# Kernel optimization log

Measured on AMD Instinct MI355X. Metric: run time of the kernel, lower is better.

The kernel has to match this reference:

```python
import jax, jax.numpy as jnp
import numpy as np

D_PRIME = 512
D = 2048
CLASSES = 4


def setup_inputs() -> dict:
    key = jax.random.key(0)
    k1, k2, k3, k4 = jax.random.split(key, 4)
    N = 32768
    V_prime = jax.random.normal(k1, (N, D), dtype=jnp.float32)
    U_t = jax.random.normal(k2, (D_PRIME, D), dtype=jnp.float32)
    W_mta = jax.random.normal(k3, (1, D_PRIME), dtype=jnp.float32)
    W = jax.random.normal(k4, (CLASSES, D), dtype=jnp.float32)
    return {"V_prime": V_prime, "U_t": U_t, "W_mta": W_mta, "W": W}


def reference(V_prime, U_t, W_mta, W):
    # [D_prime, N] = tanh(U_t @ V'^T)
    tanh_scores = jnp.tanh(U_t @ V_prime.T)
    # attention over instances: [1, N]
    a = jax.nn.softmax(W_mta @ tanh_scores, axis=1)
    # weighted sum pooling: [D]
    t = jnp.sum(a.T * V_prime, axis=0)
    # final linear: [1, classes]
    l = (W @ t).reshape(1, CLASSES)
    return l
```

## Files before the change

### kernel.cpp

```cpp
#include <hip/hip_runtime.h>

#define N_INST 32768
#define DIM    2048
#define DP     512
#define NCLS   4

typedef _Float16 half4_t __attribute__((ext_vector_type(4)));
typedef _Float16 half8_t __attribute__((ext_vector_type(8)));
typedef float    float4_t __attribute__((ext_vector_type(4)));

#define OFF_VHI   0ull
#define OFF_UHI   (OFF_VHI  + (size_t)N_INST*DIM*2)
#define OFF_S     (OFF_UHI  + (size_t)DP*DIM*2)
#define OFF_STAT  (OFF_S    + (size_t)N_INST*4)
#define OFF_PART  (OFF_STAT + 256ull)
#define OFF_T     (OFF_PART + 256ull*DIM*4)

#define GLOAD_LDS16(g, l) __builtin_amdgcn_global_load_lds( \
    (__attribute__((address_space(1))) void*)(g),           \
    (__attribute__((address_space(3))) void*)(l), 16, 0, 0)

__device__ __forceinline__ float tanh_fast(float x) {
  float e = __expf(2.0f * x);
  return 1.0f - 2.0f / (e + 1.0f);
}

__global__ __launch_bounds__(256) void k_cvt(const float4* __restrict__ in,
                                             half8_t* __restrict__ out) {
  int i = blockIdx.x * 256 + threadIdx.x;
  float4 a = in[2 * i], b = in[2 * i + 1];
  half8_t h;
  h[0] = (_Float16)a.x; h[1] = (_Float16)a.y;
  h[2] = (_Float16)a.z; h[3] = (_Float16)a.w;
  h[4] = (_Float16)b.x; h[5] = (_Float16)b.y;
  h[6] = (_Float16)b.z; h[7] = (_Float16)b.w;
  out[i] = h;
}

__global__ __launch_bounds__(256) void k_score_gemm(
    const _Float16* __restrict__ Uhi, const _Float16* __restrict__ Vhi,
    const float* __restrict__ Wmta, float* __restrict__ s) {
  __shared__ _Float16 lA[128 * 32];
  __shared__ _Float16 lB[128 * 32];

  const int tid = threadIdx.x;
  const int lane = tid & 63;
  const int wv = tid >> 6;
  const int waveM = wv >> 1;
  const int waveN = wv & 1;
  const int quad = lane >> 4;
  const int col = lane & 15;
  const int mb = blockIdx.x & 3;
  const int nb = blockIdx.x >> 2;

  const int aRow0 = mb * 128;
  const int bRow0 = nb * 128;

  float4_t acc[4][4];
  const float4_t z4 = {0.f, 0.f, 0.f, 0.f};
  for (int i = 0; i < 4; i++)
    for (int j = 0; j < 4; j++) acc[i][j] = z4;

  for (int k0 = 0; k0 < DIM; k0 += 32) {
    for (int it = 0; it < 2; ++it) {
      const int slot = it * 256 + tid;
      const int r = slot >> 2;
      const int c = (slot & 3) << 3;
      const int lbase = (it * 256 + (wv << 6)) << 3;
      GLOAD_LDS16(Uhi + (size_t)(aRow0 + r) * DIM + k0 + c, &lA[lbase]);
      GLOAD_LDS16(Vhi + (size_t)(bRow0 + r) * DIM + k0 + c, &lB[lbase]);
    }
    __syncthreads();

    half8_t af[4], bf[4];
    for (int mi = 0; mi < 4; mi++) {
      const int row = waveM * 64 + mi * 16 + col;
      af[mi] = *(const half8_t*)&lA[row * 32 + quad * 8];
    }
    for (int ni = 0; ni < 4; ni++) {
      const int row = waveN * 64 + ni * 16 + col;
      bf[ni] = *(const half8_t*)&lB[row * 32 + quad * 8];
    }
    for (int mi = 0; mi < 4; mi++)
      for (int ni = 0; ni < 4; ni++)
        acc[mi][ni] = __builtin_amdgcn_mfma_f32_16x16x32_f16(af[mi], bf[ni], acc[mi][ni], 0, 0, 0);
    __syncthreads();
  }

  for (int ni = 0; ni < 4; ni++) {
    float v = 0.0f;
    for (int mi = 0; mi < 4; mi++) {
      const int jb = aRow0 + waveM * 64 + mi * 16 + quad * 4;
      union { float4_t v4; float f[4]; } u;
      u.v4 = acc[mi][ni];
      for (int r = 0; r < 4; r++)
        v += Wmta[jb + r] * tanh_fast(u.f[r]);
    }
    v += __shfl_xor(v, 16);
    v += __shfl_xor(v, 32);
    if (quad == 0) {
      const int n = bRow0 + waveN * 64 + ni * 16 + col;
      atomicAdd(&s[n], v);
    }
  }
}

__global__ __launch_bounds__(1024) void k_stats(const float* __restrict__ s,
                                                float* __restrict__ stats) {
  const int tid = threadIdx.x;
  const int lane = tid & 63;
  const int wv = tid >> 6;
  __shared__ float sm[16];
  __shared__ float bb;
  const float4* s4 = (const float4*)s;

  float m = -3.4e38f;
  for (int i = tid; i < N_INST / 4; i += 1024) {
    float4 v = s4[i];
    m = fmaxf(m, fmaxf(fmaxf(v.x, v.y), fmaxf(v.z, v.w)));
  }
  for (int o = 32; o > 0; o >>= 1) m = fmaxf(m, __shfl_xor(m, o));
  if (lane == 0) sm[wv] = m;
  __syncthreads();
  if (tid == 0) {
    float mm = sm[0];
    for (int w = 1; w < 16; w++) mm = fmaxf(mm, sm[w]);
    bb = mm;
  }
  __syncthreads();
  const float mx = bb;

  float p = 0.0f;
  for (int i = tid; i < N_INST / 4; i += 1024) {
    float4 v = s4[i];
    p += __expf(v.x - mx) + __expf(v.y - mx) + __expf(v.z - mx) + __expf(v.w - mx);
  }
  for (int o = 32; o > 0; o >>= 1) p += __shfl_xor(p, o);
  if (lane == 0) sm[wv] = p;
  __syncthreads();
  if (tid == 0) {
    float sum = 0.0f;
    for (int w = 0; w < 16; w++) sum += sm[w];
    stats[0] = mx;
    stats[1] = 1.0f / sum;
  }
}

__global__ __launch_bounds__(256) void k_pool(const _Float16* __restrict__ Vhi,
                                              const float* __restrict__ s,
                                              const float* __restrict__ stats,
                                              float* __restrict__ part) {
  const int tid = threadIdx.x;
  const float mx = stats[0], inv = stats[1];
  const int n0 = blockIdx.x * 128;
  float acc[8] = {0.f, 0.f, 0.f, 0.f, 0.f, 0.f, 0.f, 0.f};
  for (int r = 0; r < 128; ++r) {
    const int n = n0 + r;
    const float w = __expf(s[n] - mx) * inv;
    if (w > 1e-12f) {
      half8_t v = *(const half8_t*)&Vhi[(size_t)n * DIM + tid * 8];
#pragma unroll
      for (int j = 0; j < 8; ++j) acc[j] += w * (float)v[j];
    }
  }
  float* dst = &part[(size_t)blockIdx.x * DIM + tid * 8];
  *(float4*)(dst + 0) = make_float4(acc[0], acc[1], acc[2], acc[3]);
  *(float4*)(dst + 4) = make_float4(acc[4], acc[5], acc[6], acc[7]);
}

__global__ __launch_bounds__(256) void k_reduce(const float* __restrict__ part,
                                                float* __restrict__ t) {
  const int d = blockIdx.x * 256 + threadIdx.x;
  float acc = 0.f;
  for (int b = 0; b < 256; ++b) acc += part[(size_t)b * DIM + d];
  t[d] = acc;
}

__global__ __launch_bounds__(256) void k_final(const float* __restrict__ W,
                                               const float* __restrict__ t,
                                               float* __restrict__ out) {
  const int wv = threadIdx.x >> 6;
  const int lane = threadIdx.x & 63;
  float p = 0.0f;
  for (int d = lane; d < DIM; d += 64) p += W[wv * DIM + d] * t[d];
  for (int o = 32; o > 0; o >>= 1) p += __shfl_xor(p, o);
  if (lane == 0) out[wv] = p;
}

extern "C" void kernel_launch(void* const* d_in, const int* in_sizes, int n_in,
                              void* d_out, int out_size, void* d_ws, size_t ws_size,
                              hipStream_t stream) {
  const float* Vp   = (const float*)d_in[0];
  const float* Ut   = (const float*)d_in[1];
  const float* Wmta = (const float*)d_in[2];
  const float* W    = (const float*)d_in[3];
  float* out = (float*)d_out;

  char* ws = (char*)d_ws;
  _Float16* Vhi  = (_Float16*)(ws + OFF_VHI);
  _Float16* Uhi  = (_Float16*)(ws + OFF_UHI);
  float*    sBuf = (float*)(ws + OFF_S);
  float*    stat = (float*)(ws + OFF_STAT);
  float*    partB= (float*)(ws + OFF_PART);
  float*    tBuf = (float*)(ws + OFF_T);

  hipMemsetAsync(sBuf, 0, (size_t)N_INST * 4, stream);

  k_cvt<<<(N_INST * DIM / 8) / 256, 256, 0, stream>>>((const float4*)Vp, (half8_t*)Vhi);
  k_cvt<<<(DP * DIM / 8) / 256, 256, 0, stream>>>((const float4*)Ut, (half8_t*)Uhi);
  k_score_gemm<<<(DP / 128) * (N_INST / 128), 256, 0, stream>>>(Uhi, Vhi, Wmta, sBuf);
  k_stats<<<1, 1024, 0, stream>>>(sBuf, stat);
  k_pool<<<N_INST / 128, 256, 0, stream>>>(Vhi, sBuf, stat, partB);
  k_reduce<<<DIM / 256, 256, 0, stream>>>(partB, tBuf);
  k_final<<<1, 256, 0, stream>>>(W, tBuf, out);
}
```

Before: 540.9 us.

## Fuse V fp16 conversion into score GEMM and pool, single-pass softmax stats

Removes the standalone pass that converted the large V matrix to fp16. The score GEMM now loads fp32 V tiles into swizzled LDS and converts them to fp16 in registers, and the pooling kernel reads fp32 V directly. The softmax statistics kernel computes max and sum in one online pass. This trades a full read/write of V for more bytes per GEMM tile load, double the LDS footprint for B, and more pool read traffic.

```diff
diff --git a/kernel.cpp b/kernel.cpp
--- a/kernel.cpp
+++ b/kernel.cpp
@@ -5,12 +5,10 @@
 #define DP     512
 #define NCLS   4
 
-typedef _Float16 half4_t __attribute__((ext_vector_type(4)));
 typedef _Float16 half8_t __attribute__((ext_vector_type(8)));
 typedef float    float4_t __attribute__((ext_vector_type(4)));
 
-#define OFF_VHI   0ull
-#define OFF_UHI   (OFF_VHI  + (size_t)N_INST*DIM*2)
+#define OFF_UHI   0ull
 #define OFF_S     (OFF_UHI  + (size_t)DP*DIM*2)
 #define OFF_STAT  (OFF_S    + (size_t)N_INST*4)
 #define OFF_PART  (OFF_STAT + 256ull)
@@ -38,10 +36,10 @@
 }
 
 __global__ __launch_bounds__(256) void k_score_gemm(
-    const _Float16* __restrict__ Uhi, const _Float16* __restrict__ Vhi,
+    const _Float16* __restrict__ Uhi, const float* __restrict__ V,
     const float* __restrict__ Wmta, float* __restrict__ s) {
   __shared__ _Float16 lA[128 * 32];
-  __shared__ _Float16 lB[128 * 32];
+  __shared__ float    lB[128 * 32];
 
   const int tid = threadIdx.x;
   const int lane = tid & 63;
@@ -61,14 +59,22 @@
   for (int i = 0; i < 4; i++)
     for (int j = 0; j < 4; j++) acc[i][j] = z4;
 
+  const int aR = tid >> 2;
+  const int aC = (tid & 3) << 3;
+  const int bR = tid >> 3;
+  const int bG0 = tid & 7;
+
   for (int k0 = 0; k0 < DIM; k0 += 32) {
     for (int it = 0; it < 2; ++it) {
-      const int slot = it * 256 + tid;
-      const int r = slot >> 2;
-      const int c = (slot & 3) << 3;
-      const int lbase = (it * 256 + (wv << 6)) << 3;
-      GLOAD_LDS16(Uhi + (size_t)(aRow0 + r) * DIM + k0 + c, &lA[lbase]);
-      GLOAD_LDS16(Vhi + (size_t)(bRow0 + r) * DIM + k0 + c, &lB[lbase]);
+      const int r = it * 64 + aR;
+      GLOAD_LDS16(Uhi + (size_t)(aRow0 + r) * DIM + k0 + aC,
+                  &lA[(it * 256 + (wv << 6)) << 3]);
+    }
+    for (int it = 0; it < 4; ++it) {
+      const int r = it * 32 + bR;
+      const int g = bG0 ^ (r & 7);
+      GLOAD_LDS16(V + (size_t)(bRow0 + r) * DIM + k0 + (g << 2),
+                  &lB[(it * 256 + (wv << 6)) << 2]);
     }
     __syncthreads();
 
@@ -79,7 +85,16 @@
     }
     for (int ni = 0; ni < 4; ni++) {
       const int row = waveN * 64 + ni * 16 + col;
-      bf[ni] = *(const half8_t*)&lB[row * 32 + quad * 8];
+      const int ga = (2 * quad) ^ (row & 7);
+      const int gb = (2 * quad + 1) ^ (row & 7);
+      float4_t xa = *(const float4_t*)&lB[row * 32 + ga * 4];
+      float4_t xb = *(const float4_t*)&lB[row * 32 + gb * 4];
+      half8_t b;
+      b[0] = (_Float16)xa[0]; b[1] = (_Float16)xa[1];
+      b[2] = (_Float16)xa[2]; b[3] = (_Float16)xa[3];
+      b[4] = (_Float16)xb[0]; b[5] = (_Float16)xb[1];
+      b[6] = (_Float16)xb[2]; b[7] = (_Float16)xb[3];
+      bf[ni] = b;
     }
     for (int mi = 0; mi < 4; mi++)
       for (int ni = 0; ni < 4; ni++)
@@ -109,44 +124,42 @@
                                                 float* __restrict__ stats) {
   const int tid = threadIdx.x;
   const int lane = tid & 63;
-  const int wv = tid >> 6;
-  __shared__ float sm[16];
-  __shared__ float bb;
+  const int wvi = tid >> 6;
+  __shared__ float smM[16], smP[16];
   const float4* s4 = (const float4*)s;
 
-  float m = -3.4e38f;
+  float m = -3.4e38f, p = 0.0f;
   for (int i = tid; i < N_INST / 4; i += 1024) {
     float4 v = s4[i];
-    m = fmaxf(m, fmaxf(fmaxf(v.x, v.y), fmaxf(v.z, v.w)));
-  }
-  for (int o = 32; o > 0; o >>= 1) m = fmaxf(m, __shfl_xor(m, o));
-  if (lane == 0) sm[wv] = m;
+    float xs[4] = {v.x, v.y, v.z, v.w};
+#pragma unroll
+    for (int j = 0; j < 4; ++j) {
+      float x = xs[j];
+      float nm = fmaxf(m, x);
+      p = p * __expf(m - nm) + __expf(x - nm);
+      m = nm;
+    }
+  }
+  for (int o = 32; o > 0; o >>= 1) {
+    float om = __shfl_xor(m, o);
+    float op = __shfl_xor(p, o);
+    float nm = fmaxf(m, om);
+    p = p * __expf(m - nm) + op * __expf(om - nm);
+    m = nm;
+  }
+  if (lane == 0) { smM[wvi] = m; smP[wvi] = p; }
   __syncthreads();
   if (tid == 0) {
-    float mm = sm[0];
-    for (int w = 1; w < 16; w++) mm = fmaxf(mm, sm[w]);
-    bb = mm;
-  }
-  __syncthreads();
-  const float mx = bb;
-
-  float p = 0.0f;
-  for (int i = tid; i < N_INST / 4; i += 1024) {
-    float4 v = s4[i];
-    p += __expf(v.x - mx) + __expf(v.y - mx) + __expf(v.z - mx) + __expf(v.w - mx);
-  }
-  for (int o = 32; o > 0; o >>= 1) p += __shfl_xor(p, o);
-  if (lane == 0) sm[wv] = p;
-  __syncthreads();
-  if (tid == 0) {
+    float gm = smM[0];
+    for (int w = 1; w < 16; w++) gm = fmaxf(gm, smM[w]);
     float sum = 0.0f;
-    for (int w = 0; w < 16; w++) sum += sm[w];
-    stats[0] = mx;
+    for (int w = 0; w < 16; w++) sum += smP[w] * __expf(smM[w] - gm);
+    stats[0] = gm;
     stats[1] = 1.0f / sum;
   }
 }
 
-__global__ __launch_bounds__(256) void k_pool(const _Float16* __restrict__ Vhi,
+__global__ __launch_bounds__(256) void k_pool(const float* __restrict__ V,
                                               const float* __restrict__ s,
                                               const float* __restrict__ stats,
                                               float* __restrict__ part) {
@@ -158,9 +171,10 @@
     const int n = n0 + r;
     const float w = __expf(s[n] - mx) * inv;
     if (w > 1e-12f) {
-      half8_t v = *(const half8_t*)&Vhi[(size_t)n * DIM + tid * 8];
-#pragma unroll
-      for (int j = 0; j < 8; ++j) acc[j] += w * (float)v[j];
+      const float4* vp = (const float4*)&V[(size_t)n * DIM + tid * 8];
+      float4 va = vp[0], vb = vp[1];
+      acc[0] += w * va.x; acc[1] += w * va.y; acc[2] += w * va.z; acc[3] += w * va.w;
+      acc[4] += w * vb.x; acc[5] += w * vb.y; acc[6] += w * vb.z; acc[7] += w * vb.w;
     }
   }
   float* dst = &part[(size_t)blockIdx.x * DIM + tid * 8];
@@ -179,12 +193,12 @@
 __global__ __launch_bounds__(256) void k_final(const float* __restrict__ W,
                                                const float* __restrict__ t,
                                                float* __restrict__ out) {
-  const int wv = threadIdx.x >> 6;
+  const int wvi = threadIdx.x >> 6;
   const int lane = threadIdx.x & 63;
   float p = 0.0f;
-  for (int d = lane; d < DIM; d += 64) p += W[wv * DIM + d] * t[d];
+  for (int d = lane; d < DIM; d += 64) p += W[wvi * DIM + d] * t[d];
   for (int o = 32; o > 0; o >>= 1) p += __shfl_xor(p, o);
-  if (lane == 0) out[wv] = p;
+  if (lane == 0) out[wvi] = p;
 }
 
 extern "C" void kernel_launch(void* const* d_in, const int* in_sizes, int n_in,
@@ -197,7 +211,6 @@
   float* out = (float*)d_out;
 
   char* ws = (char*)d_ws;
-  _Float16* Vhi  = (_Float16*)(ws + OFF_VHI);
   _Float16* Uhi  = (_Float16*)(ws + OFF_UHI);
   float*    sBuf = (float*)(ws + OFF_S);
   float*    stat = (float*)(ws + OFF_STAT);
@@ -206,11 +219,10 @@
 
   hipMemsetAsync(sBuf, 0, (size_t)N_INST * 4, stream);
 
-  k_cvt<<<(N_INST * DIM / 8) / 256, 256, 0, stream>>>((const float4*)Vp, (half8_t*)Vhi);
   k_cvt<<<(DP * DIM / 8) / 256, 256, 0, stream>>>((const float4*)Ut, (half8_t*)Uhi);
-  k_score_gemm<<<(DP / 128) * (N_INST / 128), 256, 0, stream>>>(Uhi, Vhi, Wmta, sBuf);
+  k_score_gemm<<<(DP / 128) * (N_INST / 128), 256, 0, stream>>>(Uhi, Vp, Wmta, sBuf);
   k_stats<<<1, 1024, 0, stream>>>(sBuf, stat);
-  k_pool<<<N_INST / 128, 256, 0, stream>>>(Vhi, sBuf, stat, partB);
+  k_pool<<<N_INST / 128, 256, 0, stream>>>(Vp, sBuf, stat, partB);
   k_reduce<<<DIM / 256, 256, 0, stream>>>(partB, tBuf);
   k_final<<<1, 256, 0, stream>>>(W, tBuf, out);
 }
```

After: 552.1 us. 2.1% more time.
